# Performance work log

Measured on AMD Instinct MI355X. Metric: run time of the kernel, lower is better.

Reference implementation:

```python
import jax, jax.numpy as jnp
import numpy as np

LATENT = 100
HID = 150
FEAT = 2
OUT = 5
B = 2048
T = 128


def setup_inputs() -> dict:
    key = jax.random.key(0)
    ks = jax.random.split(key, 16)
    k = 1.0 / np.sqrt(HID)
    u = lambda kk, shape: jax.random.uniform(kk, shape, jnp.float32, -k, k)
    return {
        "rand_noise": jax.random.normal(ks[0], (B, LATENT), jnp.float32),
        "targets": jax.random.normal(ks[1], (B, 1, FEAT), jnp.float32),
        "masks": jax.random.uniform(ks[2], (B, 1, OUT - FEAT), jnp.float32),
        "lengths": jax.random.randint(ks[3], (B,), 1, T + 1),
        "time_steps": T,
        # LSTM weights: axis 0 = direction (0 fwd, 1 bwd); gate order i,f,g,o.
        "Wih_l0": u(ks[4], (2, 4 * HID, FEAT + OUT)),
        "Whh_l0": u(ks[5], (2, 4 * HID, HID)),
        "b_l0": u(ks[6], (2, 4 * HID)),  # b_ih + b_hh combined
        "Wih_l1": u(ks[7], (2, 4 * HID, 2 * HID)),
        "Whh_l1": u(ks[8], (2, 4 * HID, HID)),
        "b_l1": u(ks[9], (2, 4 * HID)),
        "W_proj": u(ks[10], (FEAT, 2 * HID)),
        "b_proj": u(ks[11], (FEAT,)),
        "W_inith": u(ks[12], (HID * 2 * 4, LATENT + OUT)),
        "b_inith": u(ks[13], (HID * 2 * 4,)),
        "W_inittok": u(ks[14], (FEAT, LATENT + OUT)),
        "b_inittok": u(ks[15], (FEAT,)),
    }


def _cell(inp, h, c, Wih, Whh, b):
    # inp: (B, in); h, c: (B, 2, HID); weights have leading direction axis (2,...)
    g = (jnp.einsum("bi,doi->bdo", inp, Wih)
         + jnp.einsum("bdh,doh->bdo", h, Whh) + b)
    i, f, gg, o = jnp.split(g, 4, axis=-1)
    c = jax.nn.sigmoid(f) * c + jax.nn.sigmoid(i) * jnp.tanh(gg)
    h = jax.nn.sigmoid(o) * jnp.tanh(c)
    return h, c


def reference(rand_noise, targets, masks, time_steps, lengths,
              Wih_l0, Whh_l0, b_l0, Wih_l1, Whh_l1, b_l1,
              W_proj, b_proj, W_inith, b_inith, W_inittok, b_inittok):
    Bsz = rand_noise.shape[0]
    y = jnp.concatenate([targets[:, 0, :], masks[:, 0, :]], axis=-1)  # (B, OUT)
    z = jnp.concatenate([rand_noise, y], axis=-1)                     # (B, LATENT+OUT)
    # Replicates torch's (B,1200).view(8, B, 150) on the row-major buffer.
    h0c0 = (z @ W_inith.T + b_inith).reshape(8, Bsz, HID)
    h_l0 = jnp.moveaxis(h0c0[0:2], 0, 1)  # (B, 2, HID)
    h_l1 = jnp.moveaxis(h0c0[2:4], 0, 1)
    c_l0 = jnp.moveaxis(h0c0[4:6], 0, 1)
    c_l1 = jnp.moveaxis(h0c0[6:8], 0, 1)
    x = z @ W_inittok.T + b_inittok       # (B, FEAT)

    def step(carry, _):
        x, h0, c0, h1, c1 = carry
        inp = jnp.concatenate([x, y], axis=-1)           # (B, FEAT+OUT)
        h0, c0 = _cell(inp, h0, c0, Wih_l0, Whh_l0, b_l0)
        l1in = h0.reshape(Bsz, 2 * HID)                  # cat(fwd, bwd)
        h1, c1 = _cell(l1in, h1, c1, Wih_l1, Whh_l1, b_l1)
        out = h1.reshape(Bsz, 2 * HID) @ W_proj.T + b_proj  # (B, FEAT)
        return (out, h0, c0, h1, c1), out

    _, outs = jax.lax.scan(step, (x, h_l0, c_l0, h_l1, c_l1), None,
                           length=time_steps)
    outs = jnp.transpose(outs, (1, 0, 2))                # (B, T, FEAT)
    lm = (jnp.arange(time_steps)[None, :] < lengths[:, None])[..., None]
    return outs * lm.astype(outs.dtype)
```

## Files before the change

kernel.cpp:

```cpp
#include <hip/hip_runtime.h>


typedef _Float16 f16;
typedef _Float16 f16x8 __attribute__((ext_vector_type(8)));
typedef _Float16 f16x2v __attribute__((ext_vector_type(2)));
typedef float    f32x4 __attribute__((ext_vector_type(4)));

#define LOG2E 1.44269504f

__device__ __forceinline__ float sigm_(float x) {
    float e = __builtin_amdgcn_exp2f(-LOG2E * x);
    return __builtin_amdgcn_rcpf(1.f + e);
}
__device__ __forceinline__ float tanh_(float x) {
    float e = __builtin_amdgcn_exp2f(2.f * LOG2E * x);
    return 1.f - 2.f * __builtin_amdgcn_rcpf(1.f + e);
}

__device__ __forceinline__ void waitv3() {
    __builtin_amdgcn_s_waitcnt(0x0F73);
    __builtin_amdgcn_sched_barrier(0);
}
__device__ __forceinline__ void waitlgkm1() {
    __builtin_amdgcn_s_waitcnt(0xC17F);
    __builtin_amdgcn_sched_barrier(0);
}
__device__ __forceinline__ void bar_lgkm() {
    asm volatile("s_waitcnt lgkmcnt(0)" ::: "memory");
    __builtin_amdgcn_s_barrier();
    asm volatile("" ::: "memory");
}

typedef const __attribute__((address_space(1))) void* gas_t;
typedef __attribute__((address_space(3))) void* las_t;

__device__ __forceinline__ void dma_frag(const f16* wsrc, char* ringb, int F, int slot) {
    __builtin_amdgcn_global_load_lds((gas_t)(wsrc + (size_t)F * 512),
                                     (las_t)(ringb + slot * 1024), 16, 0, 0);
}

#define OFF_CINIT 2621440
#define OFF_WSTR  7864320
#define OFF_PWPJ  9502720

__device__ float dot105(const float* __restrict__ noise,
                        const float* __restrict__ targ,
                        const float* __restrict__ msk,
                        const float* __restrict__ Wrow, int bb) {
    float s = 0.f;
    const float* nz = noise + (size_t)bb * 100;
#pragma unroll 4
    for (int k = 0; k < 100; ++k) s += nz[k] * Wrow[k];
    s += targ[bb*2+0]*Wrow[100] + targ[bb*2+1]*Wrow[101];
    s += msk[bb*3+0]*Wrow[102] + msk[bb*3+1]*Wrow[103] + msk[bb*3+2]*Wrow[104];
    return s;
}

__global__ void k_init(const float* __restrict__ noise, const float* __restrict__ targ,
                       const float* __restrict__ msk,
                       const float* __restrict__ Wih, const float* __restrict__ bih,
                       const float* __restrict__ Wtk, const float* __restrict__ btk,
                       f16* __restrict__ hinit, float* __restrict__ cinitp) {
    int gid = blockIdx.x * 256 + threadIdx.x;
    int b = gid / 1280, c = gid % 1280;
    if (c < 640) {
        int reg = c / 160, loc = c % 160;
        float v = 0.f;
        if (loc < 150) {
            int q = (reg == 0) ? 3 : (reg == 1) ? 0 : (reg == 2) ? 1 : 2;
            size_t i = (size_t)q * 2048 * 150 + (size_t)b * 150 + loc;
            int bb = (int)(i / 1200), rr = (int)(i % 1200);
            v = dot105(noise, targ, msk, Wih + (size_t)rr * 105, bb) + bih[rr];
        } else if (loc == 157) {
            if (reg != 3) v = 1.0f;
        } else if (reg == 1 || reg == 2) {
            if (loc < 152) {
                int o = loc - 150;
                v = dot105(noise, targ, msk, Wtk + o * 105, b) + btk[o];
            } else if (loc == 152) v = targ[b*2+0];
            else if (loc == 153)   v = targ[b*2+1];
            else if (loc <= 156)   v = msk[b*3 + (loc - 154)];
        }
        hinit[(size_t)b * 640 + c] = (f16)v;
    } else {
        int idx = c - 640;
        int layer = idx / 320, r = idx % 320, d = r / 160, j = r % 160;
        float v = 0.f;
        if (j < 150) {
            int q = 4 + layer * 2 + d;
            size_t i = (size_t)q * 2048 * 150 + (size_t)b * 150 + j;
            int bb = (int)(i / 1200), rr = (int)(i % 1200);
            v = dot105(noise, targ, msk, Wih + (size_t)rr * 105, bb) + bih[rr];
        }
        cinitp[(((size_t)layer * 2048 + b) * 2 + d) * 160 + j] = v;
    }
}

__global__ void k_pack(const float* __restrict__ Wih0, const float* __restrict__ Whh0,
                       const float* __restrict__ bl0,
                       const float* __restrict__ Wih1, const float* __restrict__ Whh1,
                       const float* __restrict__ bl1,
                       const float* __restrict__ Wp,   const float* __restrict__ bpj,
                       f16* __restrict__ wstream, f16* __restrict__ pwpj) {
    int gid = blockIdx.x * 256 + threadIdx.x;
    if (gid < 819200) {
        int e = gid & 7, l = (gid >> 3) & 63;
        int f = (gid >> 9) % 100, w = gid / 51200;
        int r16 = l & 15, k8 = (l >> 4) * 8 + e;
        float v = 0.f;
        if (f < 25) {
            int ks = f / 5, m = f % 5;
            int mt = w * 5 + m, d = mt / 40, jt = mt % 40;
            int j = jt * 4 + (r16 >> 2), g = r16 & 3;
            int k = ks * 32 + k8;
            if (j < 150) {
                int R = d * 600 + g * 150 + j;
                if (k < 150)       v = Whh0[(size_t)R * 150 + k];
                else if (k < 157)  v = Wih0[(size_t)R * 7 + (k - 150)];
                else if (k == 157) v = bl0[R];
            }
        } else {
            int fc = f - 25, ks = fc / 5, m = fc % 5;
            int mt = w * 5 + m, d = mt / 40, jt = mt % 40;
            int j = jt * 4 + (r16 >> 2), g = r16 & 3;
            int k = ks * 32 + k8;
            if (j < 150) {
                int R = d * 600 + g * 150 + j;
                if (d == 0) {
                    if (k < 150)                  v = Wih1[(size_t)R * 300 + k];
                    else if (k == 157)            v = bl1[R];
                    else if (k >= 160 && k < 310) v = Wih1[(size_t)R * 300 + (k - 10)];
                    else if (k >= 320 && k < 470) v = Whh1[(size_t)R * 150 + (k - 320)];
                } else {
                    if (k < 150)                  v = Whh1[(size_t)R * 150 + k];
                    else if (k >= 160 && k < 310) v = Wih1[(size_t)R * 300 + (k - 160)];
                    else if (k == 317)            v = bl1[R];
                    else if (k >= 320 && k < 470) v = Wih1[(size_t)R * 300 + (k - 170)];
                }
            }
        }
        wstream[gid] = (f16)v;
    } else {
        int pg = gid - 819200;
        int e = pg & 7, l = (pg >> 3) & 63, ksi = pg >> 9;
        int ks = ksi < 5 ? ksi : ksi + 10;
        int r16 = l & 15, k = ks * 32 + (l >> 4) * 8 + e;
        float v = 0.f;
        if (r16 < 2) {
            if (k < 150)                  v = Wp[r16 * 300 + 150 + k];
            else if (k == 157)            v = bpj[r16];
            else if (k >= 480 && k < 630) v = Wp[r16 * 300 + (k - 480)];
        }
        pwpj[pg] = (f16)v;
    }
}

__global__ __launch_bounds__(1024) void lstm_main(
    const f16* __restrict__ hinit, const float* __restrict__ cinit,
    const f16* __restrict__ wstream, const f16* __restrict__ pwpj,
    const int* __restrict__ lengths, float* __restrict__ out) {
    __shared__ f16 lds[56576];
    char* ldsb = (char*)lds;
    const int tid = threadIdx.x;
    const int w = tid >> 6, l = tid & 63;
    const int b0 = blockIdx.x * 16;
    const int l15 = l & 15, lg = l >> 4;
    const int dirw = w >> 3;

    for (int it = tid; it < 16 * 80; it += 1024) {
        int row = it / 80, c8 = (it % 80) * 8;
        f16x8 v = *(const f16x8*)(hinit + (size_t)(b0 + row) * 640 + c8);
        int byte = row * 1312 + c8 * 2;  byte ^= (row & 7) << 4;
        *(f16x8*)(ldsb + byte) = v;
    }
    if (tid < 640)
        *(f16x8*)(ldsb + 20992 + tid * 16) = *(const f16x8*)(pwpj + tid * 8);

    const int jb = ((w * 5) % 40) * 4 + lg;

    float c0s[5], c1s[5];
#pragma unroll
    for (int m = 0; m < 5; ++m) {
        int b = b0 + l15;
        c0s[m] = cinit[((size_t)b * 2 + dirw) * 160 + jb + 4 * m];
        c1s[m] = cinit[(((size_t)2048 + b) * 2 + dirw) * 160 + jb + 4 * m];
    }

    int lenb = 0;
    if (w == 0 && l < 16) lenb = lengths[b0 + l];

    const int baseL0 = 160 + dirw * 160;
    const int baseL1 = dirw ? 0 : 160;
    const int hw1    = dirw ? 0 : 480;
    const f16* wsrc = wstream + (size_t)w * 51200 + l * 8;
    char* ringb = ldsb + 31232 + w * 5120;

#pragma unroll
    for (int F = 0; F < 5; ++F) dma_frag(wsrc, ringb, F, F);

    __syncthreads();

    f16x8 an = *(const f16x8*)(ringb + 0 * 1024 + l * 16);

#pragma unroll 1
    for (int t = 0; t < 128; ++t) {
        f32x4 acc[5];
#pragma unroll
        for (int m = 0; m < 5; ++m) acc[m] = (f32x4){0.f, 0.f, 0.f, 0.f};
#pragma unroll 1
        for (int ks = 0; ks < 5; ++ks) {
            int byteb = l15 * 1312 + (baseL0 + ks * 32 + lg * 8) * 2;
            byteb ^= (l15 & 7) << 4;
            f16x8 bfr = *(const f16x8*)(ldsb + byteb);
#pragma unroll
            for (int m = 0; m < 5; ++m) {
                const int F = ks * 5 + m;
                f16x8 aq = an;
                waitv3();
                an = *(const f16x8*)(ringb + ((m + 1) % 5) * 1024 + l * 16);
                waitlgkm1();
                dma_frag(wsrc, ringb, F + 5, m);
                acc[m] = __builtin_amdgcn_mfma_f32_16x16x32_f16(aq, bfr, acc[m], 0, 0, 0);
            }
        }
        bar_lgkm();
#pragma unroll
        for (int m = 0; m < 5; ++m) {
            float gi = sigm_(acc[m][0]);
            float gf = sigm_(acc[m][1]);
            float gg = tanh_(acc[m][2]);
            float go = sigm_(acc[m][3]);
            float c = gf * c0s[m] + gi * gg;
            c0s[m] = c;
            float h = go * tanh_(c);
            if (jb + 4 * m < 150) {
                int byte = l15 * 1312 + (baseL0 + jb + 4 * m) * 2;  byte ^= (l15 & 7) << 4;
                *(f16*)(ldsb + byte) = (f16)h;
            }
        }
        bar_lgkm();
#pragma unroll
        for (int m = 0; m < 5; ++m) acc[m] = (f32x4){0.f, 0.f, 0.f, 0.f};
#pragma unroll 1
        for (int ks = 0; ks < 15; ++ks) {
            int byteb = l15 * 1312 + (baseL1 + ks * 32 + lg * 8) * 2;
            byteb ^= (l15 & 7) << 4;
            f16x8 bfr = *(const f16x8*)(ldsb + byteb);
#pragma unroll
            for (int m = 0; m < 5; ++m) {
                const int F = 25 + ks * 5 + m;
                f16x8 aq = an;
                waitv3();
                an = *(const f16x8*)(ringb + ((m + 1) % 5) * 1024 + l * 16);
                waitlgkm1();
                int fr = F + 5;
                if (fr >= 100) fr -= 100;
                dma_frag(wsrc, ringb, fr, m);
                acc[m] = __builtin_amdgcn_mfma_f32_16x16x32_f16(aq, bfr, acc[m], 0, 0, 0);
            }
        }
        bar_lgkm();
#pragma unroll
        for (int m = 0; m < 5; ++m) {
            float gi = sigm_(acc[m][0]);
            float gf = sigm_(acc[m][1]);
            float gg = tanh_(acc[m][2]);
            float go = sigm_(acc[m][3]);
            float c = gf * c1s[m] + gi * gg;
            c1s[m] = c;
            float h = go * tanh_(c);
            if (jb + 4 * m < 150) {
                int byte = l15 * 1312 + (hw1 + jb + 4 * m) * 2;  byte ^= (l15 & 7) << 4;
                *(f16*)(ldsb + byte) = (f16)h;
            }
        }
        bar_lgkm();
        if (w == 0) {
            f32x4 ap = (f32x4){0.f, 0.f, 0.f, 0.f};
#pragma unroll
            for (int ksi = 0; ksi < 10; ++ksi) {
                int ks = ksi < 5 ? ksi : ksi + 10;
                int byte = l15 * 1312 + (ks * 32 + lg * 8) * 2;  byte ^= (l15 & 7) << 4;
                f16x8 bfp = *(const f16x8*)(ldsb + byte);
                f16x8 a = *(const f16x8*)(ldsb + 20992 + ksi * 1024 + l * 16);
                ap = __builtin_amdgcn_mfma_f32_16x16x32_f16(a, bfp, ap, 0, 0, 0);
            }
            if (l < 16) {
                float o0 = ap[0], o1 = ap[1];
                int b = b0 + l;
                bool live = (t < lenb);
                *(float2*)(out + ((size_t)b * 128 + t) * 2) =
                    make_float2(live ? o0 : 0.f, live ? o1 : 0.f);
                f16x2v xv = {(f16)o0, (f16)o1};
                int byte1 = l * 1312 + 620;  byte1 ^= (l & 7) << 4;
                *(f16x2v*)(ldsb + byte1) = xv;
                int byte2 = l * 1312 + 940;  byte2 ^= (l & 7) << 4;
                *(f16x2v*)(ldsb + byte2) = xv;
            }
        }
        bar_lgkm();
    }
}

extern "C" void kernel_launch(void* const* d_in, const int* in_sizes, int n_in,
                              void* d_out, int out_size, void* d_ws, size_t ws_size,
                              hipStream_t stream) {
    const float* noise = (const float*)d_in[0];
    const float* targ  = (const float*)d_in[1];
    const float* msk   = (const float*)d_in[2];
    const int*   lens  = (const int*)d_in[3];
    const float* Wih0  = (const float*)d_in[5];
    const float* Whh0  = (const float*)d_in[6];
    const float* bl0   = (const float*)d_in[7];
    const float* Wih1  = (const float*)d_in[8];
    const float* Whh1  = (const float*)d_in[9];
    const float* bl1   = (const float*)d_in[10];
    const float* Wp    = (const float*)d_in[11];
    const float* bpj   = (const float*)d_in[12];
    const float* Wit   = (const float*)d_in[13];
    const float* bit   = (const float*)d_in[14];
    const float* Wtk   = (const float*)d_in[15];
    const float* btk   = (const float*)d_in[16];

    char* ws = (char*)d_ws;
    f16*   HINIT = (f16*)(ws);
    float* CINIT = (float*)(ws + OFF_CINIT);
    f16*   WSTR  = (f16*)(ws + OFF_WSTR);
    f16*   PWPJ  = (f16*)(ws + OFF_PWPJ);

    hipLaunchKernelGGL(k_init,  dim3(10240), dim3(256), 0, stream,
                       noise, targ, msk, Wit, bit, Wtk, btk, HINIT, CINIT);
    hipLaunchKernelGGL(k_pack,  dim3(3220), dim3(256), 0, stream,
                       Wih0, Whh0, bl0, Wih1, Whh1, bl1, Wp, bpj, WSTR, PWPJ);
    hipLaunchKernelGGL(lstm_main, dim3(128), dim3(1024), 0, stream,
                       HINIT, CINIT, WSTR, PWPJ, lens, (float*)d_out);
}
```

Before: 2.070 ms.

## Stream weight fragments directly into registers instead of an LDS DMA ring

Replaces the per-wave LDS ring that was filled with global_load_lds DMA, with its manual waitcnt handling, by a five-deep register ring. Each fragment is loaded from global memory straight into VGPRs five MFMAs ahead of its use. This drops the LDS round trip and the explicit wait instructions, and shrinks the shared allocation a lot. In exchange it uses more vector registers, and the compiler now decides where to place the vmcnt waits, which could expose global memory latency.

```diff
diff --git a/kernel.cpp b/kernel.cpp
--- a/kernel.cpp
+++ b/kernel.cpp
@@ -17,26 +17,10 @@
     return 1.f - 2.f * __builtin_amdgcn_rcpf(1.f + e);
 }
 
-__device__ __forceinline__ void waitv3() {
-    __builtin_amdgcn_s_waitcnt(0x0F73);
-    __builtin_amdgcn_sched_barrier(0);
-}
-__device__ __forceinline__ void waitlgkm1() {
-    __builtin_amdgcn_s_waitcnt(0xC17F);
-    __builtin_amdgcn_sched_barrier(0);
-}
 __device__ __forceinline__ void bar_lgkm() {
     asm volatile("s_waitcnt lgkmcnt(0)" ::: "memory");
     __builtin_amdgcn_s_barrier();
     asm volatile("" ::: "memory");
-}
-
-typedef const __attribute__((address_space(1))) void* gas_t;
-typedef __attribute__((address_space(3))) void* las_t;
-
-__device__ __forceinline__ void dma_frag(const f16* wsrc, char* ringb, int F, int slot) {
-    __builtin_amdgcn_global_load_lds((gas_t)(wsrc + (size_t)F * 512),
-                                     (las_t)(ringb + slot * 1024), 16, 0, 0);
 }
 
 #define OFF_CINIT 2621440
@@ -159,7 +143,7 @@
     const f16* __restrict__ hinit, const float* __restrict__ cinit,
     const f16* __restrict__ wstream, const f16* __restrict__ pwpj,
     const int* __restrict__ lengths, float* __restrict__ out) {
-    __shared__ f16 lds[56576];
+    __shared__ f16 lds[15616];
     char* ldsb = (char*)lds;
     const int tid = threadIdx.x;
     const int w = tid >> 6, l = tid & 63;
@@ -193,14 +177,12 @@
     const int baseL1 = dirw ? 0 : 160;
     const int hw1    = dirw ? 0 : 480;
     const f16* wsrc = wstream + (size_t)w * 51200 + l * 8;
-    char* ringb = ldsb + 31232 + w * 5120;
-
-#pragma unroll
-    for (int F = 0; F < 5; ++F) dma_frag(wsrc, ringb, F, F);
+
+    f16x8 ring[5];
+#pragma unroll
+    for (int i = 0; i < 5; ++i) ring[i] = *(const f16x8*)(wsrc + (size_t)i * 512);
 
     __syncthreads();
-
-    f16x8 an = *(const f16x8*)(ringb + 0 * 1024 + l * 16);
 
 #pragma unroll 1
     for (int t = 0; t < 128; ++t) {
@@ -215,11 +197,8 @@
 #pragma unroll
             for (int m = 0; m < 5; ++m) {
                 const int F = ks * 5 + m;
-                f16x8 aq = an;
-                waitv3();
-                an = *(const f16x8*)(ringb + ((m + 1) % 5) * 1024 + l * 16);
-                waitlgkm1();
-                dma_frag(wsrc, ringb, F + 5, m);
+                f16x8 aq = ring[m];
+                ring[m] = *(const f16x8*)(wsrc + (size_t)(F + 5) * 512);
                 acc[m] = __builtin_amdgcn_mfma_f32_16x16x32_f16(aq, bfr, acc[m], 0, 0, 0);
             }
         }
@@ -246,16 +225,12 @@
             int byteb = l15 * 1312 + (baseL1 + ks * 32 + lg * 8) * 2;
             byteb ^= (l15 & 7) << 4;
             f16x8 bfr = *(const f16x8*)(ldsb + byteb);
+            int frb = 30 + ks * 5;
+            if (frb >= 100) frb -= 100;
 #pragma unroll
             for (int m = 0; m < 5; ++m) {
-                const int F = 25 + ks * 5 + m;
-                f16x8 aq = an;
-                waitv3();
-                an = *(const f16x8*)(ringb + ((m + 1) % 5) * 1024 + l * 16);
-                waitlgkm1();
-                int fr = F + 5;
-                if (fr >= 100) fr -= 100;
-                dma_frag(wsrc, ringb, fr, m);
+                f16x8 aq = ring[m];
+                ring[m] = *(const f16x8*)(wsrc + (size_t)(frb + m) * 512);
                 acc[m] = __builtin_amdgcn_mfma_f32_16x16x32_f16(aq, bfr, acc[m], 0, 0, 0);
             }
         }
```

Result: no change. 2.034 ms (median of 3 runs) (-1.7%).
